# Kernel optimization log

Measured on AMD Instinct MI355X. Metric: run time of the kernel, lower is better.

## Reference

```python
import jax, jax.numpy as jnp
import numpy as np

B, N, C, H = 8, 2048, 1024, 16
D = C // H
FOCUSING_FACTOR = 3
KERNEL = 5
EPS_BN = 1e-5


def setup_inputs() -> dict:
    key = jax.random.key(0)
    ks = jax.random.split(key, 6)
    s = lambda k, shape: jax.random.normal(k, shape, dtype=jnp.float32) * 0.02
    return {
        "hidden_states": jax.random.normal(ks[0], (B, N, C), dtype=jnp.float32),
        "bn_gamma": jnp.ones((C,), jnp.float32),
        "bn_beta": jnp.zeros((C,), jnp.float32),
        "W_qkv": s(ks[1], (C, 3 * C)),
        "b_qkv": jnp.zeros((3 * C,), jnp.float32),
        "scale_p": jnp.zeros((1, 1, C), jnp.float32),
        "dwc_w": s(ks[2], (C, 1, KERNEL)),
        "dwc_b": jnp.zeros((C,), jnp.float32),
        "W_proj": s(ks[3], (C, C)),
        "b_proj": jnp.zeros((C,), jnp.float32),
    }


def _focus(t, scale):
    # Focused feature map: relu kernel, scale, then power-3 sharpening with norm restoration
    t = jax.nn.relu(t) + 1e-6
    t = t / scale
    nrm = jnp.linalg.norm(t, axis=-1, keepdims=True)
    t = t ** FOCUSING_FACTOR
    return t / jnp.linalg.norm(t, axis=-1, keepdims=True) * nrm


def reference(hidden_states, bn_gamma, bn_beta, W_qkv, b_qkv, scale_p, dwc_w, dwc_b, W_proj, b_proj):
    x = hidden_states  # (B, N, C)
    # BatchNorm1d in training mode: per-channel stats over batch and sequence
    mean = jnp.mean(x, axis=(0, 1))
    var = jnp.mean((x - mean) ** 2, axis=(0, 1))  # biased, as torch BN uses
    xn = (x - mean) * jax.lax.rsqrt(var + EPS_BN) * bn_gamma + bn_beta

    qkv = xn @ W_qkv + b_qkv
    q, k, v = jnp.split(qkv, 3, axis=-1)
    scale = jax.nn.softplus(scale_p)
    q = _focus(q, scale)
    k = _focus(k, scale)

    heads = lambda t: t.reshape(B, N, H, D).transpose(0, 2, 1, 3)  # (B,H,N,D)
    qh, kh, vh = heads(q), heads(k), heads(v)

    # Linear attention: O(N*D^2) instead of O(N^2*D)
    z = 1.0 / (jnp.einsum('bhnd,bhd->bhn', qh, kh.sum(axis=2)) + 1e-6)
    kv = jnp.einsum('bhnd,bhne->bhde', kh, vh)  # (B,H,D,D)
    o = jnp.einsum('bhnd,bhde->bhne', qh, kv) * z[..., None]
    o = o.transpose(0, 2, 1, 3).reshape(B, N, C)

    # Depthwise conv residual on v over the sequence dim
    vc = v.transpose(0, 2, 1)  # (B,C,N)
    dwc = jax.lax.conv_general_dilated(
        vc, dwc_w, window_strides=(1,), padding=[(KERNEL // 2, KERNEL // 2)],
        dimension_numbers=('NCH', 'OIH', 'NCH'), feature_group_count=C)
    dwc = (dwc + dwc_b[None, :, None]).transpose(0, 2, 1)

    return (o + dwc) @ W_proj + b_proj
```

## Files before the change

### kernel.cpp

```cpp
#include <hip/hip_runtime.h>


#define DEV __device__ __forceinline__

typedef __attribute__((ext_vector_type(8))) short bf16x8;
typedef __attribute__((ext_vector_type(4))) float f32x4;
typedef unsigned short us;

DEV float bf2f(us u) {
  union { unsigned int i; float f; } v; v.i = ((unsigned int)u) << 16; return v.f;
}
DEV us f2bf(float f) {
  union { float f; unsigned int i; } v; v.f = f;
  unsigned int r = v.i + 0x7FFFu + ((v.i >> 16) & 1u);
  return (us)(r >> 16);
}
DEV void glds16(const us* g, us* l) {
  __builtin_amdgcn_global_load_lds((const __attribute__((address_space(1))) unsigned int*)g,
                                   (__attribute__((address_space(3))) unsigned int*)l, 16, 0, 0);
}

#define MEMFENCE asm volatile("" ::: "memory")
#define BAR do { MEMFENCE; __builtin_amdgcn_s_barrier(); MEMFENCE; } while (0)
#define LGKM0 asm volatile("s_waitcnt lgkmcnt(0)" ::: "memory")

__global__ void zero_f32(float* p, int n) {
  int i = blockIdx.x * 256 + threadIdx.x;
  if (i < n) p[i] = 0.f;
}

__global__ __launch_bounds__(256) void bn_stats(const float* __restrict__ x,
                                                float* __restrict__ s_sum, float* __restrict__ s_sq) {
  int t = threadIdx.x;
  int c0 = t * 4;
  size_t row0 = (size_t)blockIdx.x * 64;
  float s[4] = {0.f,0.f,0.f,0.f}, q[4] = {0.f,0.f,0.f,0.f};
  for (int r = 0; r < 64; ++r) {
    f32x4 v = *(const f32x4*)&x[(row0 + r) * 1024 + c0];
    #pragma unroll
    for (int i = 0; i < 4; ++i) { float f = v[i]; s[i] += f; q[i] += f * f; }
  }
  #pragma unroll
  for (int i = 0; i < 4; ++i) { atomicAdd(&s_sum[c0 + i], s[i]); atomicAdd(&s_sq[c0 + i], q[i]); }
}

__global__ void bn_finalize(const float* __restrict__ s_sum, const float* __restrict__ s_sq,
                            const float* __restrict__ gamma, const float* __restrict__ beta,
                            const float* __restrict__ scalep,
                            float* __restrict__ bn_a, float* __restrict__ bn_b, float* __restrict__ invs) {
  int c = threadIdx.x;
  float mean = s_sum[c] * (1.0f / 16384.0f);
  float var  = s_sq[c] * (1.0f / 16384.0f) - mean * mean;
  float a = gamma[c] * rsqrtf(var + 1e-5f);
  bn_a[c] = a;
  bn_b[c] = beta[c] - mean * a;
  float sv = scalep[c];
  float sp = (sv > 20.f) ? sv : log1pf(expf(sv));
  invs[c] = 1.0f / sp;
}

__global__ __launch_bounds__(256) void xn_to_bf16(const float* __restrict__ x,
                                                  const float* __restrict__ bn_a, const float* __restrict__ bn_b,
                                                  us* __restrict__ xn) {
  size_t base = ((size_t)blockIdx.x * 256 + threadIdx.x) * 8;
  int c = (int)(base & 1023);
  f32x4 a0 = *(const f32x4*)&x[base];
  f32x4 a1 = *(const f32x4*)&x[base + 4];
  uint4 o; us* uo = (us*)&o;
  #pragma unroll
  for (int i = 0; i < 4; ++i) uo[i] = f2bf(bn_a[c + i] * a0[i] + bn_b[c + i]);
  #pragma unroll
  for (int i = 0; i < 4; ++i) uo[4 + i] = f2bf(bn_a[c + 4 + i] * a1[i] + bn_b[c + 4 + i]);
  *(uint4*)&xn[base] = o;
}

__global__ __launch_bounds__(256) void transpose2(const float* __restrict__ Wqkv,
                                                  const float* __restrict__ Wproj,
                                                  us* __restrict__ outq, us* __restrict__ outp) {
  __shared__ float tile[64 * 65];
  int bx = blockIdx.x;
  const float* in; us* out; int Cc, tx;
  if (bx < 48) { in = Wqkv;  out = outq; Cc = 3072; tx = bx * 64; }
  else         { in = Wproj; out = outp; Cc = 1024; tx = (bx - 48) * 64; }
  const int R = 1024;
  int ty = blockIdx.y * 64;
  int t = threadIdx.x;
  {
    int rr = t >> 4, g = t & 15;
    #pragma unroll
    for (int p = 0; p < 4; ++p) {
      int r = p * 16 + rr;
      f32x4 v = *(const f32x4*)&in[(size_t)(ty + r) * Cc + tx + g * 4];
      #pragma unroll
      for (int i = 0; i < 4; ++i) tile[r * 65 + g * 4 + i] = v[i];
    }
  }
  __syncthreads();
  {
    int rr = t >> 3, g = t & 7;
    #pragma unroll
    for (int p = 0; p < 2; ++p) {
      int nl = p * 32 + rr;
      uint4 v; us* u = (us*)&v;
      #pragma unroll
      for (int j = 0; j < 8; ++j) u[j] = f2bf(tile[(g * 8 + j) * 65 + nl]);
      *(uint4*)&out[(size_t)(tx + nl) * R + ty + g * 8] = v;
    }
  }
}

template <typename OutT>
__global__ __launch_bounds__(512, 2) void gemm256(const us* __restrict__ A,
                                                  const us* __restrict__ Bt,
                                                  const float* __restrict__ bias,
                                                  OutT* __restrict__ Ca,
                                                  OutT* __restrict__ Cb) {
  constexpr int GK = 1024;
  __shared__ __align__(16) us As[2][2][128 * 64];
  __shared__ __align__(16) us Bs[2][2][128 * 64];
  int t = threadIdx.x;
  int wid = t >> 6, lane = t & 63;
  int l16 = lane & 15, qd = lane >> 4;
  int nwx = gridDim.x;
  int id = blockIdx.y * nwx + blockIdx.x;
  int nwg = nwx * (int)gridDim.y;
  int sw = (id & 7) * (nwg >> 3) + (id >> 3);
  int n0 = (sw % nwx) * 256, m0 = (sw / nwx) * 256;

  int rr = lane >> 3, lg = (lane & 7) ^ rr;
  const us* Asrc = A + (size_t)(m0 + wid * 8 + rr) * GK + lg * 8;
  const us* Bsrc = Bt + (size_t)(n0 + wid * 8 + rr) * GK + lg * 8;

  int wr = wid >> 2, wc = wid & 3;
  int bh = wc >> 1, brow0 = (wc & 1) * 64;

  f32x4 acc[8][4];
  const f32x4 zero4 = {0.f, 0.f, 0.f, 0.f};
  #pragma unroll
  for (int i = 0; i < 8; ++i)
    #pragma unroll
    for (int j = 0; j < 4; ++j) acc[i][j] = zero4;

  auto STAGE_A = [&](int kt, int b) {
    const us* src = Asrc + kt * 64;
    us* dst = (us*)&As[b][0][0] + wid * 512;
    #pragma unroll
    for (int g = 0; g < 4; ++g)
      glds16(src + (size_t)(g * 64) * GK, dst + g * 4096);
  };
  auto STAGE_B = [&](int kt, int b) {
    const us* src = Bsrc + kt * 64;
    us* dst = (us*)&Bs[b][0][0] + wid * 512;
    #pragma unroll
    for (int g = 0; g < 4; ++g)
      glds16(src + (size_t)(g * 64) * GK, dst + g * 4096);
  };
  auto LDA = [&](bf16x8* dst, int i0, int ks, int b) {
    #pragma unroll
    for (int i = 0; i < 4; ++i) {
      int r = (i0 + i) * 16 + l16;
      int sl = (ks * 4 + qd) ^ (r & 7);
      dst[i] = *(const bf16x8*)&As[b][wr][r * 64 + sl * 8];
    }
  };
  auto LDB = [&](bf16x8* dst, int ks, int b) {
    #pragma unroll
    for (int j = 0; j < 4; ++j) {
      int r = brow0 + j * 16 + l16;
      int sl = (ks * 4 + qd) ^ (r & 7);
      dst[j] = *(const bf16x8*)&Bs[b][bh][r * 64 + sl * 8];
    }
  };
  auto MM = [&](int i0, bf16x8* a4, bf16x8* b4) {
    __builtin_amdgcn_s_setprio(1);
    #pragma unroll
    for (int i = 0; i < 4; ++i)
      #pragma unroll
      for (int j = 0; j < 4; ++j)
        acc[i0 + i][j] = __builtin_amdgcn_mfma_f32_16x16x32_bf16(a4[i], b4[j], acc[i0 + i][j], 0, 0, 0);
    __builtin_amdgcn_s_setprio(0);
  };

  STAGE_A(0, 0); STAGE_B(0, 0);
  asm volatile("s_waitcnt vmcnt(0)" ::: "memory");
  BAR;

  for (int kt = 0; kt < 16; ++kt) {
    int buf = kt & 1, nxt = buf ^ 1;
    bf16x8 afl[4], afh[4], bfv[4];
    LDA(afl, 0, 0, buf); LDB(bfv, 0, buf);
    if (kt < 15) STAGE_A(kt + 1, nxt);
    BAR; LGKM0; MM(0, afl, bfv); BAR;
    LDA(afh, 4, 0, buf);
    if (kt < 15) STAGE_B(kt + 1, nxt);
    BAR; LGKM0; MM(4, afh, bfv); BAR;
    LDA(afl, 0, 1, buf); LDB(bfv, 1, buf);
    BAR; LGKM0; MM(0, afl, bfv); BAR;
    LDA(afh, 4, 1, buf);
    asm volatile("s_waitcnt vmcnt(0)" ::: "memory");
    BAR; LGKM0; MM(4, afh, bfv); BAR;
  }

  OutT* Cp; int col0;
  if (n0 < 1024) { Cp = Ca; col0 = n0; } else { Cp = Cb; col0 = n0 - 1024; }
  #pragma unroll
  for (int i = 0; i < 8; ++i) {
    int row = m0 + wr * 128 + i * 16 + qd * 4;
    #pragma unroll
    for (int j = 0; j < 4; ++j) {
      int fc = n0 + wc * 64 + j * 16 + l16;
      float bv = bias[fc];
      int col = col0 + wc * 64 + j * 16 + l16;
      #pragma unroll
      for (int r = 0; r < 4; ++r) {
        float val = acc[i][j][r] + bv;
        if constexpr (sizeof(OutT) == 2)
          ((us*)Cp)[(size_t)(row + r) * 1024 + col] = f2bf(val);
        else
          ((float*)Cp)[(size_t)(row + r) * 1024 + col] = val;
      }
    }
  }
}

__global__ __launch_bounds__(256) void focus_kernel(us* __restrict__ buf,
                                                    const float* __restrict__ invs) {
  int t = threadIdx.x, wid = t >> 6, lane = t & 63;
  size_t row = (size_t)blockIdx.x * 4 + wid;
  us* p = buf + row * 1024 + lane * 16;
  uint4 v0 = *(uint4*)p;
  uint4 v1 = *(uint4*)(p + 8);
  float ivv[16];
  *(f32x4*)&ivv[0]  = *(const f32x4*)&invs[lane * 16];
  *(f32x4*)&ivv[4]  = *(const f32x4*)&invs[lane * 16 + 4];
  *(f32x4*)&ivv[8]  = *(const f32x4*)&invs[lane * 16 + 8];
  *(f32x4*)&ivv[12] = *(const f32x4*)&invs[lane * 16 + 12];
  us uu[16];
  *(uint4*)&uu[0] = v0; *(uint4*)&uu[8] = v1;
  float f[16];
  float s2 = 0.f, s6 = 0.f;
  #pragma unroll
  for (int i = 0; i < 16; ++i) {
    float x = (fmaxf(bf2f(uu[i]), 0.f) + 1e-6f) * ivv[i];
    f[i] = x;
    float x2 = x * x;
    s2 += x2; s6 += x2 * x2 * x2;
  }
  #pragma unroll
  for (int off = 32; off > 0; off >>= 1) {
    s2 += __shfl_xor(s2, off);
    s6 += __shfl_xor(s6, off);
  }
  float factor = sqrtf(s2 / s6);
  #pragma unroll
  for (int i = 0; i < 16; ++i) uu[i] = f2bf(f[i] * f[i] * f[i] * factor);
  *(uint4*)p = *(uint4*)&uu[0];
  *(uint4*)(p + 8) = *(uint4*)&uu[8];
}

__global__ __launch_bounds__(256) void attn_stats3(const us* __restrict__ kbuf,
                                                   const us* __restrict__ vbuf,
                                                   float* __restrict__ ksum,
                                                   float* __restrict__ kvpart) {
  int cx = blockIdx.x, h = blockIdx.y, b = blockIdx.z, bh = b * 16 + h;
  int t = threadIdx.x, wid = t >> 6, lane = t & 63;
  int l16 = lane & 15, qd = lane >> 4;
  int wm = (wid & 1) * 32, wn = (wid >> 1) * 32;
  __shared__ __align__(16) us kT[64 * 80];
  __shared__ __align__(16) us vT[64 * 80];
  const f32x4 zero4 = {0.f, 0.f, 0.f, 0.f};
  f32x4 acc[2][2];
  #pragma unroll
  for (int i = 0; i < 2; ++i)
    #pragma unroll
    for (int j = 0; j < 2; ++j) acc[i][j] = zero4;
  float ksacc = 0.f;
  int np = (t & 31) * 2, ch0 = (t >> 5) * 8;
  int kd = t & 63, kq = t >> 6;

  for (int ck = 0; ck < 4; ++ck) {
    __syncthreads();
    size_t base = ((size_t)b * 2048 + cx * 256 + ck * 64 + np) * 1024 + h * 64 + ch0;
    uint4 k0 = *(const uint4*)&kbuf[base];
    uint4 k1 = *(const uint4*)&kbuf[base + 1024];
    uint4 v0 = *(const uint4*)&vbuf[base];
    uint4 v1 = *(const uint4*)&vbuf[base + 1024];
    us* pk0 = (us*)&k0; us* pk1 = (us*)&k1; us* pv0 = (us*)&v0; us* pv1 = (us*)&v1;
    #pragma unroll
    for (int i = 0; i < 8; ++i) {
      unsigned int pk = (unsigned int)pk0[i] | ((unsigned int)pk1[i] << 16);
      unsigned int pv = (unsigned int)pv0[i] | ((unsigned int)pv1[i] << 16);
      *(unsigned int*)&kT[(ch0 + i) * 80 + np] = pk;
      *(unsigned int*)&vT[(ch0 + i) * 80 + np] = pv;
    }
    __syncthreads();
    {
      bf16x8 ka = *(const bf16x8*)&kT[kd * 80 + kq * 16];
      bf16x8 kb = *(const bf16x8*)&kT[kd * 80 + kq * 16 + 8];
      #pragma unroll
      for (int j = 0; j < 8; ++j) ksacc += bf2f(((us*)&ka)[j]) + bf2f(((us*)&kb)[j]);
    }
    #pragma unroll
    for (int ks = 0; ks < 2; ++ks) {
      bf16x8 af[2], bfr[2];
      #pragma unroll
      for (int i = 0; i < 2; ++i) {
        af[i]  = *(const bf16x8*)&kT[(wm + i * 16 + l16) * 80 + ks * 32 + qd * 8];
        bfr[i] = *(const bf16x8*)&vT[(wn + i * 16 + l16) * 80 + ks * 32 + qd * 8];
      }
      #pragma unroll
      for (int i = 0; i < 2; ++i)
        #pragma unroll
        for (int j = 0; j < 2; ++j)
          acc[i][j] = __builtin_amdgcn_mfma_f32_16x16x32_bf16(af[i], bfr[j], acc[i][j], 0, 0, 0);
    }
  }
  float* pp = kvpart + ((size_t)cx * 128 + bh) * 4096;
  #pragma unroll
  for (int i = 0; i < 2; ++i) {
    int d = wm + i * 16 + qd * 4;
    #pragma unroll
    for (int j = 0; j < 2; ++j) {
      int e = wn + j * 16 + l16;
      #pragma unroll
      for (int r = 0; r < 4; ++r) pp[(d + r) * 64 + e] = acc[i][j][r];
    }
  }
  atomicAdd(&ksum[bh * 64 + kd], ksacc);
}

__global__ __launch_bounds__(256) void kv_reduce(const float* __restrict__ part, us* __restrict__ kvT) {
  int bh = blockIdx.x;
  int t = threadIdx.x;
  __shared__ float kvl[4096];
  #pragma unroll
  for (int p = 0; p < 16; ++p) {
    int i = p * 256 + t;
    float s = 0.f;
    #pragma unroll
    for (int c = 0; c < 8; ++c) s += part[((size_t)c * 128 + bh) * 4096 + i];
    kvl[i] = s;
  }
  __syncthreads();
  #pragma unroll
  for (int p = 0; p < 2; ++p) {
    int idx = p * 256 + t;
    int e = idx >> 3, d0 = (idx & 7) * 8;
    uint4 o; us* uo = (us*)&o;
    #pragma unroll
    for (int i = 0; i < 8; ++i) uo[i] = f2bf(kvl[(d0 + i) * 64 + e]);
    *(uint4*)&kvT[(size_t)bh * 4096 + e * 64 + d0] = o;
  }
}

__global__ __launch_bounds__(256) void attn_o2(us* __restrict__ qod,
                                               const us* __restrict__ vbuf,
                                               const float* __restrict__ ksum,
                                               const us* __restrict__ kvT,
                                               const float* __restrict__ dwcw,
                                               const float* __restrict__ dwcb) {
  int nt = blockIdx.x, h = blockIdx.y, b = blockIdx.z, bh = b * 16 + h;
  int t = threadIdx.x, wid = t >> 6, lane = t & 63;
  int l16 = lane & 15, qd = lane >> 4;
  __shared__ __align__(16) us qs[128 * 64];
  __shared__ __align__(16) us bs[64 * 64];
  __shared__ __align__(16) us vs[132 * 64];
  __shared__ float zl[128];
  __shared__ float ksl[64];
  __shared__ float wl[64 * 5];
  __shared__ float bl[64];
  int rS = t >> 3, gS = t & 7;
  size_t qbase = ((size_t)b * 2048 + nt * 128) * 1024 + h * 64;
  #pragma unroll
  for (int p = 0; p < 4; ++p) {
    int r = p * 32 + rS;
    uint4 v = *(const uint4*)&qod[qbase + (size_t)r * 1024 + gS * 8];
    *(uint4*)&qs[r * 64 + ((gS ^ (r & 7)) * 8)] = v;
  }
  #pragma unroll
  for (int p = 0; p < 2; ++p) {
    int r = p * 32 + rS;
    uint4 v = *(const uint4*)&kvT[(size_t)bh * 4096 + r * 64 + gS * 8];
    *(uint4*)&bs[r * 64 + ((gS ^ (r & 7)) * 8)] = v;
  }
  int n0 = nt * 128;
  #pragma unroll
  for (int p = 0; p < 5; ++p) {
    int idx = p * 256 + t;
    if (idx < 1056) {
      int r = idx >> 3, g = idx & 7;
      int n = n0 - 2 + r;
      uint4 v = make_uint4(0, 0, 0, 0);
      if (n >= 0 && n < 2048)
        v = *(const uint4*)&vbuf[((size_t)b * 2048 + n) * 1024 + h * 64 + g * 8];
      *(uint4*)&vs[r * 64 + g * 8] = v;
    }
  }
  if (t < 64) {
    ksl[t] = ksum[bh * 64 + t];
    bl[t] = dwcb[h * 64 + t];
    #pragma unroll
    for (int j = 0; j < 5; ++j) wl[t * 5 + j] = dwcw[(h * 64 + t) * 5 + j];
  }
  __syncthreads();
  if (t < 128) {
    float zs = 0.f;
    #pragma unroll
    for (int g = 0; g < 8; ++g) {
      bf16x8 qv = *(const bf16x8*)&qs[t * 64 + ((g ^ (t & 7)) * 8)];
      #pragma unroll
      for (int j = 0; j < 8; ++j) zs += bf2f(((us*)&qv)[j]) * ksl[g * 8 + j];
    }
    zl[t] = 1.f / (zs + 1e-6f);
  }
  __syncthreads();
  const f32x4 zero4 = {0.f, 0.f, 0.f, 0.f};
  f32x4 acc[2][4];
  #pragma unroll
  for (int i = 0; i < 2; ++i)
    #pragma unroll
    for (int j = 0; j < 4; ++j) acc[i][j] = zero4;
  #pragma unroll
  for (int ks = 0; ks < 2; ++ks) {
    bf16x8 af[2], bfr[4];
    #pragma unroll
    for (int i = 0; i < 2; ++i) {
      int ml = (wid * 2 + i) * 16 + l16;
      af[i] = *(const bf16x8*)&qs[ml * 64 + (((ks * 4 + qd) ^ (ml & 7)) * 8)];
    }
    #pragma unroll
    for (int j = 0; j < 4; ++j) {
      int nl = j * 16 + l16;
      bfr[j] = *(const bf16x8*)&bs[nl * 64 + (((ks * 4 + qd) ^ (nl & 7)) * 8)];
    }
    #pragma unroll
    for (int i = 0; i < 2; ++i)
      #pragma unroll
      for (int j = 0; j < 4; ++j)
        acc[i][j] = __builtin_amdgcn_mfma_f32_16x16x32_bf16(af[i], bfr[j], acc[i][j], 0, 0, 0);
  }
  #pragma unroll
  for (int i = 0; i < 2; ++i) {
    int rl0 = (wid * 2 + i) * 16 + qd * 4;
    #pragma unroll
    for (int j = 0; j < 4; ++j) {
      int e = j * 16 + l16;
      float w0 = wl[e * 5], w1 = wl[e * 5 + 1], w2 = wl[e * 5 + 2], w3 = wl[e * 5 + 3], w4 = wl[e * 5 + 4];
      float vv[8];
      #pragma unroll
      for (int m = 0; m < 8; ++m) vv[m] = bf2f(vs[(rl0 + m) * 64 + e]);
      float bb = bl[e];
      #pragma unroll
      for (int r = 0; r < 4; ++r) {
        float dwc = vv[r] * w0 + vv[r + 1] * w1 + vv[r + 2] * w2 + vv[r + 3] * w3 + vv[r + 4] * w4;
        float o = acc[i][j][r] * zl[rl0 + r] + dwc + bb;
        qod[qbase + (size_t)(rl0 + r) * 1024 + e] = f2bf(o);
      }
    }
  }
}

extern "C" void kernel_launch(void* const* d_in, const int* in_sizes, int n_in,
                              void* d_out, int out_size, void* d_ws, size_t ws_size,
                              hipStream_t stream) {
  const float* x      = (const float*)d_in[0];
  const float* gamma  = (const float*)d_in[1];
  const float* beta   = (const float*)d_in[2];
  const float* Wqkv   = (const float*)d_in[3];
  const float* bqkv   = (const float*)d_in[4];
  const float* scalep = (const float*)d_in[5];
  const float* dwcw   = (const float*)d_in[6];
  const float* dwcb   = (const float*)d_in[7];
  const float* Wproj  = (const float*)d_in[8];
  const float* bproj  = (const float*)d_in[9];
  float* out = (float*)d_out;

  float* wsf = (float*)d_ws;
  float* s_sum  = wsf;
  float* s_sq   = wsf + 1024;
  float* ksum   = wsf + 2048;
  float* bn_a   = wsf + 10240;
  float* bn_b   = wsf + 11264;
  float* invs   = wsf + 12288;
  float* kvpart = wsf + 13312;
  us* kvT = (us*)(wsf + 4207616);
  us* wtq = (us*)(wsf + 4469760);
  us* wtp = (us*)(wsf + 6042624);
  us* kq  = (us*)(wsf + 6566912);
  us* vbf = (us*)d_out;
  us* xnb = (us*)d_out + 16777216;

  zero_f32<<<40, 256, 0, stream>>>(wsf, 10240);
  bn_stats<<<256, 256, 0, stream>>>(x, s_sum, s_sq);
  bn_finalize<<<1, 1024, 0, stream>>>(s_sum, s_sq, gamma, beta, scalep, bn_a, bn_b, invs);
  xn_to_bf16<<<8192, 256, 0, stream>>>(x, bn_a, bn_b, xnb);
  transpose2<<<dim3(64, 16), 256, 0, stream>>>(Wqkv, Wproj, wtq, wtp);

  gemm256<us><<<dim3(8, 64), 512, 0, stream>>>(xnb, wtq + 1024 * 1024, bqkv + 1024, kq, vbf);
  focus_kernel<<<4096, 256, 0, stream>>>(kq, invs);
  attn_stats3<<<dim3(8, 16, 8), 256, 0, stream>>>(kq, vbf, ksum, kvpart);
  kv_reduce<<<128, 256, 0, stream>>>(kvpart, kvT);
  gemm256<us><<<dim3(4, 64), 512, 0, stream>>>(xnb, wtq, bqkv, kq, kq);
  focus_kernel<<<4096, 256, 0, stream>>>(kq, invs);
  attn_o2<<<dim3(16, 16, 8), 256, 0, stream>>>(kq, vbf, ksum, kvT, dwcw, dwcb);
  gemm256<float><<<dim3(4, 64), 512, 0, stream>>>(kq, wtp, bproj, out, out);
}
```

Baseline: 387.4 us.

## Halve GEMM K-tile to 32 to cut LDS and raise occupancy

```diff
diff --git a/kernel.cpp b/kernel.cpp
--- a/kernel.cpp
+++ b/kernel.cpp
@@ -110,14 +110,14 @@
 }
 
 template <typename OutT>
-__global__ __launch_bounds__(512, 2) void gemm256(const us* __restrict__ A,
+__global__ __launch_bounds__(512, 4) void gemm256(const us* __restrict__ A,
                                                   const us* __restrict__ Bt,
                                                   const float* __restrict__ bias,
                                                   OutT* __restrict__ Ca,
                                                   OutT* __restrict__ Cb) {
   constexpr int GK = 1024;
-  __shared__ __align__(16) us As[2][2][128 * 64];
-  __shared__ __align__(16) us Bs[2][2][128 * 64];
+  __shared__ __align__(16) us As[2][128 * 64];
+  __shared__ __align__(16) us Bs[2][128 * 64];
   int t = threadIdx.x;
   int wid = t >> 6, lane = t & 63;
   int l16 = lane & 15, qd = lane >> 4;
@@ -127,12 +127,13 @@
   int sw = (id & 7) * (nwg >> 3) + (id >> 3);
   int n0 = (sw % nwx) * 256, m0 = (sw / nwx) * 256;
 
-  int rr = lane >> 3, lg = (lane & 7) ^ rr;
-  const us* Asrc = A + (size_t)(m0 + wid * 8 + rr) * GK + lg * 8;
-  const us* Bsrc = Bt + (size_t)(n0 + wid * 8 + rr) * GK + lg * 8;
+  int rr = lane >> 3, sl = lane & 7;
+  int lg = sl ^ rr;
+  int grp = lg >> 2, ch = lg & 3;
+  const us* Asrc = A + (size_t)(m0 + wid * 8 + rr + 128 * grp) * GK + ch * 8;
+  const us* Bsrc = Bt + (size_t)(n0 + wid * 8 + rr + 128 * grp) * GK + ch * 8;
 
   int wr = wid >> 2, wc = wid & 3;
-  int bh = wc >> 1, brow0 = (wc & 1) * 64;
 
   f32x4 acc[8][4];
   const f32x4 zero4 = {0.f, 0.f, 0.f, 0.f};
@@ -142,33 +143,32 @@
     for (int j = 0; j < 4; ++j) acc[i][j] = zero4;
 
   auto STAGE_A = [&](int kt, int b) {
-    const us* src = Asrc + kt * 64;
-    us* dst = (us*)&As[b][0][0] + wid * 512;
-    #pragma unroll
-    for (int g = 0; g < 4; ++g)
-      glds16(src + (size_t)(g * 64) * GK, dst + g * 4096);
+    const us* src = Asrc + (size_t)kt * 32;
+    us* dst = (us*)&As[b][0] + (wid * 8) * 64;
+    glds16(src, dst);
+    glds16(src + (size_t)64 * GK, dst + 64 * 64);
   };
   auto STAGE_B = [&](int kt, int b) {
-    const us* src = Bsrc + kt * 64;
-    us* dst = (us*)&Bs[b][0][0] + wid * 512;
-    #pragma unroll
-    for (int g = 0; g < 4; ++g)
-      glds16(src + (size_t)(g * 64) * GK, dst + g * 4096);
+    const us* src = Bsrc + (size_t)kt * 32;
+    us* dst = (us*)&Bs[b][0] + (wid * 8) * 64;
+    glds16(src, dst);
+    glds16(src + (size_t)64 * GK, dst + 64 * 64);
   };
-  auto LDA = [&](bf16x8* dst, int i0, int ks, int b) {
+  auto LDA = [&](bf16x8* d4, int i0, int b) {
     #pragma unroll
     for (int i = 0; i < 4; ++i) {
       int r = (i0 + i) * 16 + l16;
-      int sl = (ks * 4 + qd) ^ (r & 7);
-      dst[i] = *(const bf16x8*)&As[b][wr][r * 64 + sl * 8];
+      int ps = (wr * 4 + qd) ^ (r & 7);
+      d4[i] = *(const bf16x8*)((const us*)&As[b][0] + r * 64 + ps * 8);
     }
   };
-  auto LDB = [&](bf16x8* dst, int ks, int b) {
+  auto LDB = [&](bf16x8* d4, int b) {
     #pragma unroll
     for (int j = 0; j < 4; ++j) {
-      int r = brow0 + j * 16 + l16;
-      int sl = (ks * 4 + qd) ^ (r & 7);
-      dst[j] = *(const bf16x8*)&Bs[b][bh][r * 64 + sl * 8];
+      int rowb = wc * 64 + j * 16 + l16;
+      int grpb = rowb >> 7, rb = rowb & 127;
+      int ps = (grpb * 4 + qd) ^ (rb & 7);
+      d4[j] = *(const bf16x8*)((const us*)&Bs[b][0] + rb * 64 + ps * 8);
     }
   };
   auto MM = [&](int i0, bf16x8* a4, bf16x8* b4) {
@@ -185,18 +185,13 @@
   asm volatile("s_waitcnt vmcnt(0)" ::: "memory");
   BAR;
 
-  for (int kt = 0; kt < 16; ++kt) {
+  for (int kt = 0; kt < 32; ++kt) {
     int buf = kt & 1, nxt = buf ^ 1;
     bf16x8 afl[4], afh[4], bfv[4];
-    LDA(afl, 0, 0, buf); LDB(bfv, 0, buf);
-    if (kt < 15) STAGE_A(kt + 1, nxt);
+    LDA(afl, 0, buf); LDB(bfv, buf);
+    if (kt < 31) { STAGE_A(kt + 1, nxt); STAGE_B(kt + 1, nxt); }
     BAR; LGKM0; MM(0, afl, bfv); BAR;
-    LDA(afh, 4, 0, buf);
-    if (kt < 15) STAGE_B(kt + 1, nxt);
-    BAR; LGKM0; MM(4, afh, bfv); BAR;
-    LDA(afl, 0, 1, buf); LDB(bfv, 1, buf);
-    BAR; LGKM0; MM(0, afl, bfv); BAR;
-    LDA(afh, 4, 1, buf);
+    LDA(afh, 4, buf);
     asm volatile("s_waitcnt vmcnt(0)" ::: "memory");
     BAR; LGKM0; MM(4, afh, bfv); BAR;
   }
```

Result: slower. 1.354 ms (+249.6%).
